# Optimization experiments

Measured on AMD Instinct MI355X. Metric: run time of the kernel, lower is better.

The kernel has to match this reference:

```python
import jax, jax.numpy as jnp
import numpy as np

RADIUS = 0.1
NSAMPLE = 32
B, N, NPOINT, C = 2, 16384, 4096, 64


def setup_inputs() -> dict:
    key = jax.random.key(0)
    k1, k2, k3 = jax.random.split(key, 3)
    xyz = jax.random.uniform(k1, (B, N, 3), dtype=jnp.float32)
    new_xyz = jax.random.uniform(k2, (B, NPOINT, 3), dtype=jnp.float32)
    features = jax.random.normal(k3, (B, C, N), dtype=jnp.float32)
    return {"xyz": xyz, "new_xyz": new_xyz, "features": features}


def ball_query(radius, nsample, xyz, new_xyz):
    # xyz: (B, N, 3), new_xyz: (B, npoint, 3) -> idx: (B, npoint, nsample) int32
    # Semantics of the CUDA ball_query: take the first `nsample` points (in
    # original order) whose squared distance < radius^2; pad remaining slots
    # with the first in-ball index (0 if the ball is empty).
    d2 = jnp.sum((new_xyz[:, :, None, :] - xyz[:, None, :, :]) ** 2, axis=-1)  # (B, npoint, N)
    mask = d2 < radius * radius
    # stable argsort puts in-ball indices first, preserving original order
    order = jnp.argsort(jnp.where(mask, 0, 1), axis=-1)  # (B, npoint, N)
    cnt = jnp.sum(mask, axis=-1, keepdims=True)  # (B, npoint, 1)
    first = jnp.where(cnt > 0, order[..., :1], 0)  # (B, npoint, 1)
    slots = jnp.arange(nsample)
    idx = jnp.where(slots < cnt, order[..., :nsample], first)
    return idx.astype(jnp.int32)


def group(features, idx):
    # features: (B, C, N), idx: (B, npoint, nsample) -> (B, C, npoint, nsample)
    return jax.vmap(lambda f, i: f[:, i])(features, idx)


def reference(xyz, new_xyz, features):
    idx = ball_query(RADIUS, NSAMPLE, xyz, new_xyz)  # (B, npoint, nsample)
    xyz_t = jnp.transpose(xyz, (0, 2, 1))  # (B, 3, N)
    grouped_xyz = group(xyz_t, idx)  # (B, 3, npoint, nsample)
    grouped_xyz = grouped_xyz - jnp.transpose(new_xyz, (0, 2, 1))[..., None]
    grouped_features = group(features, idx)  # (B, C, npoint, nsample)
    new_features = jnp.concatenate([grouped_xyz, grouped_features], axis=1)
    return new_features  # (B, 3 + C, npoint, nsample)
```

## Files before the change

### kernel.cpp

```cpp
#include <hip/hip_runtime.h>

#define B 2
#define N 16384
#define NPOINT 4096
#define C 64
#define NSAMPLE 32

#define NCELL 1000
#define CELLW_STRIDE 1024
#define OFF_STRIDE 1056
#define CAP 192

#define BALL_BLOCKS (B * NPOINT / 4)
#define TRANS_BLOCKS (B * (N / 64))

__device__ __forceinline__ float r2_thresh() { return (float)(0.1 * 0.1); }

__device__ __forceinline__ int clamp09(int v) { return v < 0 ? 0 : (v > 9 ? 9 : v); }

__device__ __forceinline__ int cell_of(float x, float y, float z) {
    const int ix = clamp09((int)floorf(x * 10.0f));
    const int iy = clamp09((int)floorf(y * 10.0f));
    const int iz = clamp09((int)floorf(z * 10.0f));
    return (ix * 10 + iy) * 10 + iz;
}

__global__ void __launch_bounds__(256) grid_hist_kernel(
    const float* __restrict__ xyz, const float* __restrict__ new_xyz,
    int* __restrict__ cellwork, int* __restrict__ qwork) {
    const int i = blockIdx.x * blockDim.x + threadIdx.x;
    if (i < B * N) {
        const int b = i / N;
        const float x = xyz[(size_t)i * 3 + 0];
        const float y = xyz[(size_t)i * 3 + 1];
        const float z = xyz[(size_t)i * 3 + 2];
        atomicAdd(&cellwork[b * CELLW_STRIDE + cell_of(x, y, z)], 1);
    } else if (i < B * (N + NPOINT)) {
        const int qi = i - B * N;
        const int b = qi / NPOINT;
        const float x = new_xyz[(size_t)qi * 3 + 0];
        const float y = new_xyz[(size_t)qi * 3 + 1];
        const float z = new_xyz[(size_t)qi * 3 + 2];
        atomicAdd(&qwork[b * CELLW_STRIDE + cell_of(x, y, z)], 1);
    }
}

__global__ void __launch_bounds__(1024) grid_scan_kernel(
    int* __restrict__ cellwork, int* __restrict__ qwork, int* __restrict__ off) {
    __shared__ int wsum[16];
    const int blk = blockIdx.x;
    const int t = threadIdx.x;
    const int lane = t & 63;
    const int w = t >> 6;
    int* __restrict__ arr = (blk < B) ? (cellwork + blk * CELLW_STRIDE)
                                      : (qwork + (blk - B) * CELLW_STRIDE);
    const int v = (t < NCELL) ? arr[t] : 0;

    int s = v;
#pragma unroll
    for (int d = 1; d < 64; d <<= 1) {
        const int u = __shfl_up(s, d, 64);
        if (lane >= d) s += u;
    }
    if (lane == 63) wsum[w] = s;
    __syncthreads();
    if (w == 0) {
        int p = (lane < 16) ? wsum[lane] : 0;
#pragma unroll
        for (int d = 1; d < 16; d <<= 1) {
            const int u = __shfl_up(p, d, 64);
            if (lane >= d) p += u;
        }
        if (lane < 16) wsum[lane] = p;
    }
    __syncthreads();
    const int prefix = (w > 0) ? wsum[w - 1] : 0;
    const int excl = s + prefix - v;
    if (blk < B && t <= NCELL) off[blk * OFF_STRIDE + t] = excl;
    if (t < NCELL) arr[t] = excl;
}

__global__ void __launch_bounds__(256) grid_scatter_kernel(
    const float* __restrict__ xyz, const float* __restrict__ new_xyz,
    int* __restrict__ cellwork, int* __restrict__ qwork,
    float4* __restrict__ binned, int* __restrict__ qperm) {
    const int i = blockIdx.x * blockDim.x + threadIdx.x;
    if (i < B * N) {
        const int b = i / N;
        const int p = i - b * N;
        const float x = xyz[(size_t)i * 3 + 0];
        const float y = xyz[(size_t)i * 3 + 1];
        const float z = xyz[(size_t)i * 3 + 2];
        const int c = cell_of(x, y, z);
        const int pos = atomicAdd(&cellwork[b * CELLW_STRIDE + c], 1);
        float4 v;
        v.x = x; v.y = y; v.z = z; v.w = __int_as_float(p);
        binned[(size_t)b * N + pos] = v;
    } else if (i < B * (N + NPOINT)) {
        const int qi = i - B * N;
        const int b = qi / NPOINT;
        const int j = qi - b * NPOINT;
        const float x = new_xyz[(size_t)qi * 3 + 0];
        const float y = new_xyz[(size_t)qi * 3 + 1];
        const float z = new_xyz[(size_t)qi * 3 + 2];
        const int c = cell_of(x, y, z);
        const int pos = atomicAdd(&qwork[b * CELLW_STRIDE + c], 1);
        qperm[b * NPOINT + pos] = j;
    }
}

__device__ void linear_ball_fallback(const float* __restrict__ xb,
                                     float cx, float cy, float cz,
                                     int lane, unsigned long long lanemask_lt,
                                     int* out) {
    const float r2 = r2_thresh();
    int cnt = 0, first_idx = 0;
    for (int base = 0; base < N; base += 64) {
        const int i = base + lane;
        const float x = xb[i * 3 + 0];
        const float y = xb[i * 3 + 1];
        const float z = xb[i * 3 + 2];
        float d2;
        {
#pragma clang fp contract(off)
            float dx = x - cx;
            float dy = y - cy;
            float dz = z - cz;
            d2 = dx * dx + dy * dy + dz * dz;
        }
        const bool in = d2 < r2;
        const unsigned long long m = __ballot(in);
        if (in) {
            const int pos = cnt + __popcll(m & lanemask_lt);
            if (pos < NSAMPLE) out[pos] = i;
        }
        if (cnt == 0 && m != 0ull) first_idx = base + __builtin_ctzll(m);
        cnt += __popcll(m);
        if (cnt >= NSAMPLE) break;
    }
    if (cnt < NSAMPLE) {
        if (cnt == 0) first_idx = 0;
        for (int pos = cnt + lane; pos < NSAMPLE; pos += 64) out[pos] = first_idx;
    }
}

__device__ __forceinline__ void rank_select(const int* cand, int K, int lane,
                                            int* __restrict__ out) {
    const int e0 = (lane < K) ? cand[lane] : 0x7FFFFFFF;
    const int e1 = (64 + lane < K) ? cand[64 + lane] : 0x7FFFFFFF;
    const int e2 = (128 + lane < K) ? cand[128 + lane] : 0x7FFFFFFF;
    int r0 = 0, r1 = 0, r2i = 0;
    if (K <= 64) {
        for (int k = 0; k < K; ++k) { const int v = cand[k]; r0 += (v < e0); }
    } else if (K <= 128) {
        for (int k = 0; k < K; ++k) { const int v = cand[k]; r0 += (v < e0); r1 += (v < e1); }
    } else {
        for (int k = 0; k < K; ++k) {
            const int v = cand[k];
            r0 += (v < e0); r1 += (v < e1); r2i += (v < e2);
        }
    }
    if (lane < K && r0 < NSAMPLE) out[r0] = e0;
    if (64 + lane < K && r1 < NSAMPLE) out[r1] = e1;
    if (128 + lane < K && r2i < NSAMPLE) out[r2i] = e2;

    if (K < NSAMPLE) {
        int mn = min(e0, min(e1, e2));
#pragma unroll
        for (int d = 32; d; d >>= 1) mn = min(mn, __shfl_xor(mn, d));
        const int fill = (K > 0) ? mn : 0;
        for (int pos = K + lane; pos < NSAMPLE; pos += 64) out[pos] = fill;
    }
}

__device__ __forceinline__ int scan_window(
    const float4* __restrict__ bb, const int* __restrict__ ob,
    int lox, int hix, int loy, int hiy, int loz, int hiz,
    float cx, float cy, float cz, int lane,
    unsigned long long lanemask_lt, int* cand)
{
    const float r2 = r2_thresh();
    int K = 0;
    for (int ix = lox; ix <= hix; ++ix) {
        for (int iy = loy; iy <= hiy; ++iy) {
            const int rowc = (ix * 10 + iy) * 10;
            const int s0 = ob[rowc + loz];
            const int s1 = ob[rowc + hiz + 1];
            for (int cur = s0; cur < s1; cur += 64) {
                const int i = cur + lane;
                const bool valid = (i < s1);
                float4 pv;
                if (valid) pv = bb[i];
                else { pv.x = 1e9f; pv.y = 1e9f; pv.z = 1e9f; pv.w = 0.0f; }
                float d2;
                {
#pragma clang fp contract(off)
                    float dx = pv.x - cx, dy = pv.y - cy, dz = pv.z - cz;
                    d2 = dx * dx + dy * dy + dz * dz;
                }
                const bool in = valid && (d2 < r2);
                const unsigned long long m = __ballot(in);
                if (in) {
                    const int pos = K + __popcll(m & lanemask_lt);
                    if (pos < CAP) cand[pos] = __float_as_int(pv.w);
                }
                K += __popcll(m);
            }
        }
    }
    return K;
}

__global__ void __launch_bounds__(256) ball_and_transpose_kernel(
    const float4* __restrict__ binned,
    const int* __restrict__ off,
    const float* __restrict__ new_xyz,
    const float* __restrict__ xyz,
    const int* __restrict__ qperm,
    int* __restrict__ idx_out,
    const float* __restrict__ feat,
    float* __restrict__ ft)
{
    __shared__ int cand_s[4][CAP];
    __shared__ float tile[64 * 65];

    const int t = threadIdx.x;

    if (blockIdx.x >= BALL_BLOCKS) {
        const int tb = blockIdx.x - BALL_BLOCKS;
        const int b = tb / (N / 64);
        const int n0 = (tb % (N / 64)) * 64;
        const int l = t & 63;
        const int w = t >> 6;
#pragma unroll
        for (int it = 0; it < 16; ++it) {
            const int c = it * 4 + w;
            tile[c * 65 + l] = feat[((size_t)b * C + c) * N + n0 + l];
        }
        __syncthreads();
#pragma unroll
        for (int it = 0; it < 16; ++it) {
            const int nn = it * 4 + w;
            ft[((size_t)b * N + n0 + nn) * C + l] = tile[l * 65 + nn];
        }
        return;
    }

    const int lane = t & 63;
    const int wib = t >> 6;
    const int wave = blockIdx.x * 4 + wib;
    const int b = wave / NPOINT;
    const int sp = wave - b * NPOINT;
    const int j = qperm[b * NPOINT + sp];

    const float cx = new_xyz[((size_t)b * NPOINT + j) * 3 + 0];
    const float cy = new_xyz[((size_t)b * NPOINT + j) * 3 + 1];
    const float cz = new_xyz[((size_t)b * NPOINT + j) * 3 + 2];

    int* cand = cand_s[wib];
    const float4* __restrict__ bb = binned + (size_t)b * N;
    const int* __restrict__ ob = off + b * OFF_STRIDE;
    int* __restrict__ out = idx_out + ((size_t)b * NPOINT + j) * NSAMPLE;

    const unsigned long long lanemask_lt = (lane == 63) ? 0x7FFFFFFFFFFFFFFFull
                                                        : ((1ull << lane) - 1ull);

    const int lox = max(0, (int)floorf((cx - 0.1001f) * 10.0f));
    const int hix = min(9, (int)floorf((cx + 0.1001f) * 10.0f));
    const int loy = max(0, (int)floorf((cy - 0.1001f) * 10.0f));
    const int hiy = min(9, (int)floorf((cy + 0.1001f) * 10.0f));
    const int loz = max(0, (int)floorf((cz - 0.1001f) * 10.0f));
    const int hiz = min(9, (int)floorf((cz + 0.1001f) * 10.0f));

    const int K = scan_window(bb, ob, lox, hix, loy, hiy, loz, hiz,
                              cx, cy, cz, lane, lanemask_lt, cand);

    if (K > CAP) {
        linear_ball_fallback(xyz + (size_t)b * N * 3, cx, cy, cz, lane, lanemask_lt, out);
    } else {
        rank_select(cand, K, lane, out);
    }
}

__global__ void __launch_bounds__(256) group2_kernel(
    const float* __restrict__ xyz, const float* __restrict__ new_xyz,
    const float* __restrict__ ft, const int* __restrict__ idx_arr,
    const int* __restrict__ qperm, float* __restrict__ out) {
    __shared__ int sidx[64];
    __shared__ float sf[64 * 65];

    const int t = threadIdx.x;
    const int g = blockIdx.x;
    const int nwg = B * NPOINT / 2;
    const int swz = (g & 7) * (nwg / 8) + (g >> 3);
    const int b = swz / (NPOINT / 2);
    const int p = swz - b * (NPOINT / 2);

    const int q0 = qperm[b * NPOINT + 2 * p + 0];
    const int q1 = qperm[b * NPOINT + 2 * p + 1];

    if (t < 64) {
        const int qq = (t < 32) ? q0 : q1;
        sidx[t] = idx_arr[((size_t)b * NPOINT + qq) * NSAMPLE + (t & 31)];
    }
    __syncthreads();

    {
        const int lane16 = t & 15;
        const int pq = t >> 4;
#pragma unroll
        for (int it = 0; it < 4; ++it) {
            const int pp = it * 16 + pq;
            const int id = sidx[pp];
            const float4 v = *(const float4*)(ft + ((size_t)b * N + id) * C + lane16 * 4);
            float* dst = sf + pp * 65 + lane16 * 4;
            dst[0] = v.x; dst[1] = v.y; dst[2] = v.z; dst[3] = v.w;
        }
    }

    const size_t plane = (size_t)NPOINT * NSAMPLE;
    const size_t bbase = (size_t)b * (3 + C) * plane;

    if (t < 64) {
        const int id = sidx[t];
        const int qq = (t < 32) ? q0 : q1;
        const size_t cb = ((size_t)b * NPOINT + qq) * 3;
        const size_t pb = ((size_t)b * N + id) * 3;
        const size_t ob = bbase + (size_t)qq * NSAMPLE + (t & 31);
        {
#pragma clang fp contract(off)
            out[ob + 0 * plane] = xyz[pb + 0] - new_xyz[cb + 0];
            out[ob + 1 * plane] = xyz[pb + 1] - new_xyz[cb + 1];
            out[ob + 2 * plane] = xyz[pb + 2] - new_xyz[cb + 2];
        }
    }
    __syncthreads();

    const int l = t & 63;
    const int w = t >> 6;
    const int qq = (l < 32) ? q0 : q1;
    const size_t rowbase = bbase + (size_t)qq * NSAMPLE + (l & 31);
#pragma unroll
    for (int it = 0; it < 16; ++it) {
        const int c = it * 4 + w;
        out[rowbase + (size_t)(3 + c) * plane] = sf[l * 65 + c];
    }
}

__global__ void __launch_bounds__(256) ball_query_kernel(
    const float* __restrict__ xyz, const float* __restrict__ new_xyz,
    int* __restrict__ idx_out)
{
    const int wave = (blockIdx.x * blockDim.x + threadIdx.x) >> 6;
    const int lane = threadIdx.x & 63;
    if (wave >= B * NPOINT) return;
    const int b = wave / NPOINT;
    const float cx = new_xyz[(size_t)wave * 3 + 0];
    const float cy = new_xyz[(size_t)wave * 3 + 1];
    const float cz = new_xyz[(size_t)wave * 3 + 2];
    const unsigned long long lanemask_lt = (lane == 63) ? 0x7FFFFFFFFFFFFFFFull
                                                        : ((1ull << lane) - 1ull);
    linear_ball_fallback(xyz + (size_t)b * N * 3, cx, cy, cz, lane, lanemask_lt,
                         idx_out + (size_t)wave * NSAMPLE);
}

__global__ void __launch_bounds__(256) group_kernel(
    const float* __restrict__ xyz, const float* __restrict__ new_xyz,
    const float* __restrict__ feat, const int* __restrict__ idx_arr,
    float* __restrict__ out) {
    const int t = threadIdx.x;
    const int s = t & 31;
    const int jl = t >> 5;
    const int j = blockIdx.x * 8 + jl;
    const int b = blockIdx.y;

    const int id = idx_arr[((size_t)b * NPOINT + j) * NSAMPLE + s];

    const float px = xyz[((size_t)b * N + id) * 3 + 0] - new_xyz[((size_t)b * NPOINT + j) * 3 + 0];
    const float py = xyz[((size_t)b * N + id) * 3 + 1] - new_xyz[((size_t)b * NPOINT + j) * 3 + 1];
    const float pz = xyz[((size_t)b * N + id) * 3 + 2] - new_xyz[((size_t)b * NPOINT + j) * 3 + 2];

    const size_t plane = (size_t)NPOINT * NSAMPLE;
    const size_t obase = (size_t)b * (3 + C) * plane + (size_t)j * NSAMPLE + s;

    out[obase + 0 * plane] = px;
    out[obase + 1 * plane] = py;
    out[obase + 2 * plane] = pz;

    const float* __restrict__ fb = feat + (size_t)b * C * N;
#pragma unroll 8
    for (int c = 0; c < C; ++c) {
        out[obase + (size_t)(3 + c) * plane] = fb[(size_t)c * N + id];
    }
}

extern "C" void kernel_launch(void* const* d_in, const int* in_sizes, int n_in,
                              void* d_out, int out_size, void* d_ws, size_t ws_size,
                              hipStream_t stream) {
    const float* xyz     = (const float*)d_in[0];
    const float* new_xyz = (const float*)d_in[1];
    const float* feat    = (const float*)d_in[2];
    float* out = (float*)d_out;

    const size_t idx_bytes    = (size_t)B * NPOINT * NSAMPLE * sizeof(int);
    const size_t ft_bytes     = (size_t)B * N * C * sizeof(float);
    const size_t binned_bytes = (size_t)B * N * sizeof(float4);
    const size_t off_bytes    = (size_t)B * OFF_STRIDE * sizeof(int);
    const size_t cellw_bytes  = (size_t)B * CELLW_STRIDE * sizeof(int);
    const size_t qwork_bytes  = (size_t)B * CELLW_STRIDE * sizeof(int);
    const size_t qperm_bytes  = (size_t)B * NPOINT * sizeof(int);

    char* ws = (char*)d_ws;
    size_t o = 0;
    int*    idx_ws   = (int*)(ws + o);    o += idx_bytes;
    float*  ft       = (float*)(ws + o);  o += ft_bytes;
    float4* binned   = (float4*)(ws + o); o += binned_bytes;
    int*    off      = (int*)(ws + o);    o += off_bytes;
    int*    cellwork = (int*)(ws + o);    o += cellw_bytes;
    int*    qwork    = (int*)(ws + o);    o += qwork_bytes;
    int*    qperm    = (int*)(ws + o);    o += qperm_bytes;

    const bool use_grid = (ws_size >= o);

    if (use_grid) {
        hipMemsetAsync(cellwork, 0, cellw_bytes + qwork_bytes, stream);
        grid_hist_kernel<<<(B * (N + NPOINT) + 255) / 256, 256, 0, stream>>>(
            xyz, new_xyz, cellwork, qwork);
        grid_scan_kernel<<<2 * B, 1024, 0, stream>>>(cellwork, qwork, off);
        grid_scatter_kernel<<<(B * (N + NPOINT) + 255) / 256, 256, 0, stream>>>(
            xyz, new_xyz, cellwork, qwork, binned, qperm);
        ball_and_transpose_kernel<<<BALL_BLOCKS + TRANS_BLOCKS, 256, 0, stream>>>(
            binned, off, new_xyz, xyz, qperm, idx_ws, feat, ft);
        group2_kernel<<<B * NPOINT / 2, 256, 0, stream>>>(
            xyz, new_xyz, ft, idx_ws, qperm, out);
    } else {
        ball_query_kernel<<<(B * NPOINT) / 4, 256, 0, stream>>>(xyz, new_xyz, idx_ws);
        dim3 grid2(NPOINT / 8, B);
        group_kernel<<<grid2, 256, 0, stream>>>(xyz, new_xyz, feat, idx_ws, out);
    }
}
```

Before: 52.55 us.

## Fuse ball query with grouping and move feature transpose into histogram kernel

The feature transpose moves out of the ball-query launch and into the histogram kernel as extra blocks. Ball query and grouping become one kernel: each block finds neighbors for four queries into shared memory, then gathers features and writes the output directly. This removes the global idx round-trip and one kernel launch. In exchange, the fused block uses more shared memory and runs an imbalanced ball-query phase before the gather, which may hurt occupancy and overlap.

```diff
diff --git a/kernel.cpp b/kernel.cpp
--- a/kernel.cpp
+++ b/kernel.cpp
@@ -11,7 +11,7 @@
 #define OFF_STRIDE 1056
 #define CAP 192
 
-#define BALL_BLOCKS (B * NPOINT / 4)
+#define HIST_BLOCKS ((B * (N + NPOINT) + 255) / 256)
 #define TRANS_BLOCKS (B * (N / 64))
 
 __device__ __forceinline__ float r2_thresh() { return (float)(0.1 * 0.1); }
@@ -25,10 +25,34 @@
     return (ix * 10 + iy) * 10 + iz;
 }
 
-__global__ void __launch_bounds__(256) grid_hist_kernel(
+__global__ void __launch_bounds__(256) hist_transpose_kernel(
     const float* __restrict__ xyz, const float* __restrict__ new_xyz,
-    int* __restrict__ cellwork, int* __restrict__ qwork) {
-    const int i = blockIdx.x * blockDim.x + threadIdx.x;
+    int* __restrict__ cellwork, int* __restrict__ qwork,
+    const float* __restrict__ feat, float* __restrict__ ft) {
+    __shared__ float tile[64 * 65];
+    const int t = threadIdx.x;
+
+    if (blockIdx.x >= HIST_BLOCKS) {
+        const int tb = blockIdx.x - HIST_BLOCKS;
+        const int b = tb / (N / 64);
+        const int n0 = (tb % (N / 64)) * 64;
+        const int l = t & 63;
+        const int w = t >> 6;
+#pragma unroll
+        for (int it = 0; it < 16; ++it) {
+            const int c = it * 4 + w;
+            tile[c * 65 + l] = feat[((size_t)b * C + c) * N + n0 + l];
+        }
+        __syncthreads();
+#pragma unroll
+        for (int it = 0; it < 16; ++it) {
+            const int nn = it * 4 + w;
+            ft[((size_t)b * N + n0 + nn) * C + l] = tile[l * 65 + nn];
+        }
+        return;
+    }
+
+    const int i = blockIdx.x * blockDim.x + t;
     if (i < B * N) {
         const int b = i / N;
         const float x = xyz[(size_t)i * 3 + 0];
@@ -145,7 +169,7 @@
 }
 
 __device__ __forceinline__ void rank_select(const int* cand, int K, int lane,
-                                            int* __restrict__ out) {
+                                            int* out) {
     const int e0 = (lane < K) ? cand[lane] : 0x7FFFFFFF;
     const int e1 = (64 + lane < K) ? cand[64 + lane] : 0x7FFFFFFF;
     const int e2 = (128 + lane < K) ? cand[128 + lane] : 0x7FFFFFFF;
@@ -211,56 +235,41 @@
     return K;
 }
 
-__global__ void __launch_bounds__(256) ball_and_transpose_kernel(
+__global__ void __launch_bounds__(256) fused_kernel(
     const float4* __restrict__ binned,
     const int* __restrict__ off,
     const float* __restrict__ new_xyz,
     const float* __restrict__ xyz,
+    const float* __restrict__ ft,
     const int* __restrict__ qperm,
-    int* __restrict__ idx_out,
-    const float* __restrict__ feat,
-    float* __restrict__ ft)
+    float* __restrict__ out)
 {
     __shared__ int cand_s[4][CAP];
-    __shared__ float tile[64 * 65];
+    __shared__ int sidx[4 * NSAMPLE];
+    __shared__ int sj[4];
+    __shared__ float sf[64 * 65];
 
     const int t = threadIdx.x;
-
-    if (blockIdx.x >= BALL_BLOCKS) {
-        const int tb = blockIdx.x - BALL_BLOCKS;
-        const int b = tb / (N / 64);
-        const int n0 = (tb % (N / 64)) * 64;
-        const int l = t & 63;
-        const int w = t >> 6;
-#pragma unroll
-        for (int it = 0; it < 16; ++it) {
-            const int c = it * 4 + w;
-            tile[c * 65 + l] = feat[((size_t)b * C + c) * N + n0 + l];
-        }
-        __syncthreads();
-#pragma unroll
-        for (int it = 0; it < 16; ++it) {
-            const int nn = it * 4 + w;
-            ft[((size_t)b * N + n0 + nn) * C + l] = tile[l * 65 + nn];
-        }
-        return;
-    }
-
     const int lane = t & 63;
-    const int wib = t >> 6;
-    const int wave = blockIdx.x * 4 + wib;
-    const int b = wave / NPOINT;
-    const int sp = wave - b * NPOINT;
-    const int j = qperm[b * NPOINT + sp];
+    const int w = t >> 6;
+
+    const int nwg = B * NPOINT / 4;
+    const int g = blockIdx.x;
+    const int swz = (g & 7) * (nwg / 8) + (g >> 3);
+    const int b = swz / (NPOINT / 4);
+    const int p4 = swz % (NPOINT / 4);
+
+    const int j = qperm[b * NPOINT + p4 * 4 + w];
+    if (lane == 0) sj[w] = j;
 
     const float cx = new_xyz[((size_t)b * NPOINT + j) * 3 + 0];
     const float cy = new_xyz[((size_t)b * NPOINT + j) * 3 + 1];
     const float cz = new_xyz[((size_t)b * NPOINT + j) * 3 + 2];
 
-    int* cand = cand_s[wib];
+    int* cand = cand_s[w];
+    int* sout = sidx + w * NSAMPLE;
     const float4* __restrict__ bb = binned + (size_t)b * N;
     const int* __restrict__ ob = off + b * OFF_STRIDE;
-    int* __restrict__ out = idx_out + ((size_t)b * NPOINT + j) * NSAMPLE;
 
     const unsigned long long lanemask_lt = (lane == 63) ? 0x7FFFFFFFFFFFFFFFull
                                                         : ((1ull << lane) - 1ull);
@@ -276,74 +285,54 @@
                               cx, cy, cz, lane, lanemask_lt, cand);
 
     if (K > CAP) {
-        linear_ball_fallback(xyz + (size_t)b * N * 3, cx, cy, cz, lane, lanemask_lt, out);
+        linear_ball_fallback(xyz + (size_t)b * N * 3, cx, cy, cz, lane, lanemask_lt, sout);
     } else {
-        rank_select(cand, K, lane, out);
-    }
-}
-
-__global__ void __launch_bounds__(256) group2_kernel(
-    const float* __restrict__ xyz, const float* __restrict__ new_xyz,
-    const float* __restrict__ ft, const int* __restrict__ idx_arr,
-    const int* __restrict__ qperm, float* __restrict__ out) {
-    __shared__ int sidx[64];
-    __shared__ float sf[64 * 65];
-
-    const int t = threadIdx.x;
-    const int g = blockIdx.x;
-    const int nwg = B * NPOINT / 2;
-    const int swz = (g & 7) * (nwg / 8) + (g >> 3);
-    const int b = swz / (NPOINT / 2);
-    const int p = swz - b * (NPOINT / 2);
-
-    const int q0 = qperm[b * NPOINT + 2 * p + 0];
-    const int q1 = qperm[b * NPOINT + 2 * p + 1];
-
-    if (t < 64) {
-        const int qq = (t < 32) ? q0 : q1;
-        sidx[t] = idx_arr[((size_t)b * NPOINT + qq) * NSAMPLE + (t & 31)];
+        rank_select(cand, K, lane, sout);
     }
     __syncthreads();
-
-    {
-        const int lane16 = t & 15;
-        const int pq = t >> 4;
-#pragma unroll
-        for (int it = 0; it < 4; ++it) {
-            const int pp = it * 16 + pq;
-            const int id = sidx[pp];
-            const float4 v = *(const float4*)(ft + ((size_t)b * N + id) * C + lane16 * 4);
-            float* dst = sf + pp * 65 + lane16 * 4;
-            dst[0] = v.x; dst[1] = v.y; dst[2] = v.z; dst[3] = v.w;
-        }
-    }
 
     const size_t plane = (size_t)NPOINT * NSAMPLE;
     const size_t bbase = (size_t)b * (3 + C) * plane;
 
-    if (t < 64) {
+    if (t < 128) {
         const int id = sidx[t];
-        const int qq = (t < 32) ? q0 : q1;
-        const size_t cb = ((size_t)b * NPOINT + qq) * 3;
+        const int jq = sj[t >> 5];
+        const int s = t & 31;
+        const size_t cb = ((size_t)b * NPOINT + jq) * 3;
         const size_t pb = ((size_t)b * N + id) * 3;
-        const size_t ob = bbase + (size_t)qq * NSAMPLE + (t & 31);
+        const size_t obx = bbase + (size_t)jq * NSAMPLE + s;
         {
 #pragma clang fp contract(off)
-            out[ob + 0 * plane] = xyz[pb + 0] - new_xyz[cb + 0];
-            out[ob + 1 * plane] = xyz[pb + 1] - new_xyz[cb + 1];
-            out[ob + 2 * plane] = xyz[pb + 2] - new_xyz[cb + 2];
-        }
-    }
-    __syncthreads();
-
-    const int l = t & 63;
-    const int w = t >> 6;
-    const int qq = (l < 32) ? q0 : q1;
-    const size_t rowbase = bbase + (size_t)qq * NSAMPLE + (l & 31);
-#pragma unroll
-    for (int it = 0; it < 16; ++it) {
-        const int c = it * 4 + w;
-        out[rowbase + (size_t)(3 + c) * plane] = sf[l * 65 + c];
+            out[obx + 0 * plane] = xyz[pb + 0] - new_xyz[cb + 0];
+            out[obx + 1 * plane] = xyz[pb + 1] - new_xyz[cb + 1];
+            out[obx + 2 * plane] = xyz[pb + 2] - new_xyz[cb + 2];
+        }
+    }
+
+#pragma unroll
+    for (int h = 0; h < 2; ++h) {
+        const int* sidxL = sidx + h * 64;
+        {
+            const int lane16 = t & 15;
+            const int pg = t >> 4;
+#pragma unroll
+            for (int it = 0; it < 4; ++it) {
+                const int pp = it * 16 + pg;
+                const int id = sidxL[pp];
+                const float4 v = *(const float4*)(ft + ((size_t)b * N + id) * C + lane16 * 4);
+                float* dst = sf + pp * 65 + lane16 * 4;
+                dst[0] = v.x; dst[1] = v.y; dst[2] = v.z; dst[3] = v.w;
+            }
+        }
+        __syncthreads();
+        const int q = sj[2 * h + (lane >> 5)];
+        const size_t rowbase = bbase + (size_t)q * NSAMPLE + (lane & 31);
+#pragma unroll
+        for (int it = 0; it < 16; ++it) {
+            const int c = it * 4 + w;
+            out[rowbase + (size_t)(3 + c) * plane] = sf[lane * 65 + c];
+        }
+        __syncthreads();
     }
 }
 
@@ -424,15 +413,13 @@
 
     if (use_grid) {
         hipMemsetAsync(cellwork, 0, cellw_bytes + qwork_bytes, stream);
-        grid_hist_kernel<<<(B * (N + NPOINT) + 255) / 256, 256, 0, stream>>>(
-            xyz, new_xyz, cellwork, qwork);
+        hist_transpose_kernel<<<HIST_BLOCKS + TRANS_BLOCKS, 256, 0, stream>>>(
+            xyz, new_xyz, cellwork, qwork, feat, ft);
         grid_scan_kernel<<<2 * B, 1024, 0, stream>>>(cellwork, qwork, off);
         grid_scatter_kernel<<<(B * (N + NPOINT) + 255) / 256, 256, 0, stream>>>(
             xyz, new_xyz, cellwork, qwork, binned, qperm);
-        ball_and_transpose_kernel<<<BALL_BLOCKS + TRANS_BLOCKS, 256, 0, stream>>>(
-            binned, off, new_xyz, xyz, qperm, idx_ws, feat, ft);
-        group2_kernel<<<B * NPOINT / 2, 256, 0, stream>>>(
-            xyz, new_xyz, ft, idx_ws, qperm, out);
+        fused_kernel<<<B * NPOINT / 4, 256, 0, stream>>>(
+            binned, off, new_xyz, xyz, ft, qperm, out);
     } else {
         ball_query_kernel<<<(B * NPOINT) / 4, 256, 0, stream>>>(xyz, new_xyz, idx_ws);
         dim3 grid2(NPOINT / 8, B);
```

Measured after the change: 46.86 us. 10.8% less time.
